# Performance work log

Measured on AMD Instinct MI355X. Metric: run time of the kernel, lower is better.

The kernel has to match this reference:

```python
import jax, jax.numpy as jnp
import numpy as np

B, C, H, W = 16, 64, 32, 32
E, HEADS, FF, L = 64, 4, 256, 3
NO_UNIT, INB = 6, 58
LN_EPS = 1e-5


def setup_inputs() -> dict:
    key = jax.random.key(0)
    ks = jax.random.split(key, 16)
    x = jax.random.normal(ks[0], (B, C, H, W), jnp.float32)
    # channel 58 = in-bounds everywhere; channel 6 = no-unit flag (Bernoulli 0.5)
    x = x.at[:, INB].set(1.0)
    x = x.at[:, NO_UNIT].set(jax.random.bernoulli(ks[1], 0.5, (B, H, W)).astype(jnp.float32))
    s = 0.05
    return {
        'x': x,
        'embed_w': jax.random.normal(ks[2], (C + 2, E), jnp.float32) * s,
        'embed_b': jnp.zeros((E,), jnp.float32),
        'ln1_w': jnp.ones((L, E), jnp.float32),
        'ln1_b': jnp.zeros((L, E), jnp.float32),
        'in_proj_w': jax.random.normal(ks[3], (L, 3 * E, E), jnp.float32) * s,
        'in_proj_b': jnp.zeros((L, 3 * E), jnp.float32),
        'out_w': jax.random.normal(ks[4], (L, E, E), jnp.float32) * s,
        'out_b': jnp.zeros((L, E), jnp.float32),
        'ln2_w': jnp.ones((L, E), jnp.float32),
        'ln2_b': jnp.zeros((L, E), jnp.float32),
        'ff1_w': jax.random.normal(ks[5], (L, E, FF), jnp.float32) * s,
        'ff1_b': jnp.zeros((L, FF), jnp.float32),
        'ff2_w': jax.random.normal(ks[6], (L, FF, E), jnp.float32) * s,
        'ff2_b': jnp.zeros((L, E), jnp.float32),
    }


def _layer_norm(x, w, b):
    mu = jnp.mean(x, axis=-1, keepdims=True)
    var = jnp.mean(jnp.square(x - mu), axis=-1, keepdims=True)
    return (x - mu) * jax.lax.rsqrt(var + LN_EPS) * w + b


def reference(x, embed_w, embed_b, ln1_w, ln1_b, in_proj_w, in_proj_b,
              out_w, out_b, ln2_w, ln2_b, ff1_w, ff1_b, ff2_w, ff2_b):
    Bn, Cn, Hn, Wn = x.shape
    S = Hn * Wn
    # position features (H == W here, matching torch tile/t() layout)
    ly = jnp.linspace(-1.0, 1.0, Hn)
    lx = jnp.linspace(-1.0, 1.0, Wn)
    pos = jnp.stack([jnp.tile(ly, (Wn, 1)), jnp.tile(lx, (Hn, 1)).T], axis=0)  # [2,H,W]
    xf = jnp.concatenate([x, jnp.broadcast_to(pos, (Bn, 2, Hn, Wn))], axis=1)
    xs = xf.reshape(Bn, Cn + 2, S).transpose(0, 2, 1)  # [B,S,C+2]

    # empty-space mask + vectorized squash (stable sort packs kept tokens first)
    empty = (xs[..., NO_UNIT] != 0) & (xs[..., INB] != 0)  # True = empty/masked
    keep = ~empty
    order = jnp.argsort(empty.astype(jnp.int32), axis=1, stable=True)  # [B,S]
    x_sq = jnp.take_along_axis(xs, order[:, :, None], axis=1)  # [B,S,C+2]
    n_keep = jnp.sum(keep, axis=1)
    pad = jnp.arange(S)[None, :] >= n_keep[:, None]  # True = padded key
    # (torch squashes to max(n_keep); padding to S is mathematically identical
    #  since padded rows are masked as keys and discarded on unsquash)
    bias = jnp.where(pad, -1e30, 0.0)[:, None, None, :]  # [B,1,1,S]

    h = x_sq @ embed_w + embed_b  # [B,S,E]
    dh = E // HEADS
    scale = 1.0 / float(np.sqrt(dh))
    for l in range(L):
        # identity_map_reordering: pre-norm attention
        a_in = _layer_norm(h, ln1_w[l], ln1_b[l])
        qkv = a_in @ in_proj_w[l].T + in_proj_b[l]
        q, k, v = jnp.split(qkv, 3, axis=-1)
        q = q.reshape(Bn, S, HEADS, dh)
        k = k.reshape(Bn, S, HEADS, dh)
        v = v.reshape(Bn, S, HEADS, dh)
        scores = jnp.einsum('bqhd,bkhd->bhqk', q, k) * scale + bias
        attn = jax.nn.softmax(scores, axis=-1)
        o = jnp.einsum('bhqk,bkhd->bqhd', attn, v).reshape(Bn, S, E)
        h = h + (o @ out_w[l].T + out_b[l])
        # pre-norm feed-forward (exact GELU, as nn.GELU default)
        f_in = _layer_norm(h, ln2_w[l], ln2_b[l])
        ff = jax.nn.gelu(f_in @ ff1_w[l] + ff1_b[l], approximate=False) @ ff2_w[l] + ff2_b[l]
        h = h + ff

    # unsquash: inverse permutation, zero at empty positions
    inv = jnp.argsort(order, axis=1)
    out = jnp.take_along_axis(h, inv[:, :, None], axis=1) * keep[:, :, None].astype(h.dtype)
    return out.transpose(0, 2, 1).reshape(Bn, E, Hn, Wn)
```

## Files before the change

kernel.cpp:

```cpp
#include <hip/hip_runtime.h>


#define BB 16
#define SS 1024
#define NT (BB*SS)

typedef short bf8 __attribute__((ext_vector_type(8)));
typedef float f4 __attribute__((ext_vector_type(4)));
typedef unsigned short u16;
typedef unsigned short us4 __attribute__((ext_vector_type(4)));

#define MFMA(a,b,c) __builtin_amdgcn_mfma_f32_16x16x32_bf16(a,b,c,0,0,0)

__device__ __forceinline__ float b2f(u16 u){
  union { unsigned int i; float f; } v; v.i = ((unsigned int)u) << 16; return v.f;
}
__device__ __forceinline__ u16 f2b(float f){
  union { float f; unsigned int i; } v; v.f = f;
  unsigned int x = v.i;
  return (u16)((x + 0x7FFFu + ((x >> 16) & 1u)) >> 16);
}
__device__ __forceinline__ int probe_f32(const void* ln1w){
  return ((const u16*)ln1w)[0] == 0;
}
__device__ __forceinline__ float ldf(const void* p, int i, int isf32){
  return isf32 ? ((const float*)p)[i] : b2f(((const u16*)p)[i]);
}
__device__ __forceinline__ bf8 ldbf8(const void* p, int idx, int isf32){
  if (!isf32) return *(const bf8*)((const u16*)p + idx);
  const float* s = (const float*)p + idx;
  bf8 r;
  #pragma unroll
  for (int j = 0; j < 8; j++) r[j] = (short)f2b(s[j]);
  return r;
}
__device__ __forceinline__ float gelu(float x){
  float y = 1.5957691216f * x * (1.f + 0.044715f * x * x);
  float e = __expf(y);
  return x - x * __builtin_amdgcn_rcpf(e + 1.f);
}

#define O_L1W  64
#define O_L1B  256
#define O_IPW  448
#define O_IPB  37312
#define O_OW   37888
#define O_OWB  50176
#define O_L2W  50368
#define O_L2B  50560
#define O_F1B  50752
#define O_F2B  51520

__device__ __forceinline__ void cv(u16* dst, const void* src, int n, int isf32,
                                   int tid, int nth){
  if (isf32){
    const float* s = (const float*)src;
    for (int i = tid; i < n; i += nth) dst[i] = f2b(s[i]);
  } else {
    const u16* s = (const u16*)src;
    for (int i = tid; i < n; i += nth) dst[i] = s[i];
  }
}

__device__ __forceinline__ void qkv_core(bf8 a0, bf8 a1, bf8 b0, bf8 b1,
    int j, float bj, int lane, int bb4, int sw,
    u16* __restrict__ qb, u16* __restrict__ kb, u16* __restrict__ vt)
{
  int quad = lane >> 4;
  f4 acc = {0.f,0.f,0.f,0.f};
  acc = MFMA(a0, b0, acc);
  acc = MFMA(a1, b1, acc);
  if (j < 128){
    u16* dst = (j < 64) ? qb : kb;
    int jj = j & 63; int hd = jj >> 4, d = jj & 15;
    int base = (bb4 + hd)*1024 + sw + quad*4;
    #pragma unroll
    for (int r = 0; r < 4; r++) dst[((base + r) << 4) + d] = f2b(acc[r] + bj);
  } else {
    int jj = j - 128; int hd = jj >> 4, d = jj & 15;
    us4 pk;
    #pragma unroll
    for (int r = 0; r < 4; r++) pk[r] = f2b(acc[r] + bj);
    *(us4*)(vt + ((bb4 + hd)*16 + d)*1024 + sw + quad*4) = pk;
  }
}

__device__ __forceinline__ void ln_to_lds(const f4* hf, int lane,
    const u16* __restrict__ w, const u16* __restrict__ bs, u16* als)
{
  int col = lane & 15, quad = lane >> 4;
  float sm[4], sq[4];
  #pragma unroll
  for (int r = 0; r < 4; r++){
    float a = 0.f, q2 = 0.f;
    #pragma unroll
    for (int f = 0; f < 4; f++){ float v = hf[f][r]; a += v; q2 += v*v; }
    sm[r] = a; sq[r] = q2;
  }
  #pragma unroll
  for (int off = 1; off < 16; off <<= 1){
    #pragma unroll
    for (int r = 0; r < 4; r++){
      sm[r] += __shfl_xor(sm[r], off, 64);
      sq[r] += __shfl_xor(sq[r], off, 64);
    }
  }
  #pragma unroll
  for (int r = 0; r < 4; r++){
    float m = sm[r] * 0.015625f;
    float rstd = rsqrtf(fmaxf(sq[r]*0.015625f - m*m, 0.f) + 1e-5f);
    sm[r] = m; sq[r] = rstd;
  }
  #pragma unroll
  for (int f = 0; f < 4; f++){
    int n = f*16 + col;
    float ww = b2f(w[n]), bb = b2f(bs[n]);
    #pragma unroll
    for (int r = 0; r < 4; r++)
      als[(quad*4 + r)*72 + n] = f2b((hf[f][r] - sm[r])*sq[r]*ww + bb);
  }
}

__device__ __forceinline__ void ln4(f4 val, int wave, int col, int quad,
    const u16* __restrict__ w, const u16* __restrict__ bs,
    u16* als, float (*lnred)[16][2])
{
  float sm[4], sq[4];
  #pragma unroll
  for (int r = 0; r < 4; r++){ sm[r] = val[r]; sq[r] = val[r]*val[r]; }
  #pragma unroll
  for (int off = 1; off < 16; off <<= 1){
    #pragma unroll
    for (int r = 0; r < 4; r++){
      sm[r] += __shfl_xor(sm[r], off, 64);
      sq[r] += __shfl_xor(sq[r], off, 64);
    }
  }
  if (col == 0){
    #pragma unroll
    for (int r = 0; r < 4; r++){
      lnred[wave][quad*4 + r][0] = sm[r];
      lnred[wave][quad*4 + r][1] = sq[r];
    }
  }
  __syncthreads();
  int n = wave*16 + col;
  float ww = b2f(w[n]), bb = b2f(bs[n]);
  #pragma unroll
  for (int r = 0; r < 4; r++){
    int row = quad*4 + r;
    float s0 = lnred[0][row][0] + lnred[1][row][0] + lnred[2][row][0] + lnred[3][row][0];
    float q0 = lnred[0][row][1] + lnred[1][row][1] + lnred[2][row][1] + lnred[3][row][1];
    float m = s0 * 0.015625f;
    float rs = rsqrtf(fmaxf(q0*0.015625f - m*m, 0.f) + 1e-5f);
    als[row*72 + n] = f2b((val[r] - m)*rs*ww + bb);
  }
}

__global__ __launch_bounds__(256) void k0(
    const void* __restrict__ x,    const void* __restrict__ ewS,
    const void* __restrict__ ebS,  const void* __restrict__ l1wS,
    const void* __restrict__ l1bS, const void* __restrict__ ipwS,
    const void* __restrict__ ipbS, const void* __restrict__ owS,
    const void* __restrict__ owbS, const void* __restrict__ l2wS,
    const void* __restrict__ l2bS, const void* __restrict__ f1wS,
    const void* __restrict__ f1bS, const void* __restrict__ f2wS,
    const void* __restrict__ f2bS,
    u16* __restrict__ cb, u16* __restrict__ f1t, u16* __restrict__ f2t,
    float* __restrict__ h, float* __restrict__ keepf,
    u16* __restrict__ qb, u16* __restrict__ kb, u16* __restrict__ vt)
{
  __shared__ __align__(16) u16 xs[4][16*104];
  __shared__ __align__(16) u16 als[4][16*72];
  __shared__ __align__(16) u16 ews[64*96];
  __shared__ __align__(16) u16 wsm[384];
  int tid = threadIdx.x;
  int lane = tid & 63, wave = tid >> 6;
  int col = lane & 15, quad = lane >> 4;
  int isf32 = probe_f32(l1wS);

  {
    int gtid = blockIdx.x*256 + tid;
    int nth  = gridDim.x*256;
    for (int i = gtid; i < 3*256*64; i += nth){
      int l = i / (256*64); int r = i % (256*64); int n = r / 64, k = r % 64;
      f1t[i] = f2b(ldf(f1wS, (l*64 + k)*256 + n, isf32));
    }
    for (int i = gtid; i < 3*64*256; i += nth){
      int l = i / (64*256); int r = i % (64*256); int n = r / 256, k = r % 256;
      f2t[i] = f2b(ldf(f2wS, (l*256 + k)*64 + n, isf32));
    }
    cv(cb + O_L1W, l1wS, 192,   isf32, gtid, nth);
    cv(cb + O_L1B, l1bS, 192,   isf32, gtid, nth);
    cv(cb + O_IPW, ipwS, 36864, isf32, gtid, nth);
    cv(cb + O_IPB, ipbS, 576,   isf32, gtid, nth);
    cv(cb + O_OW,  owS,  12288, isf32, gtid, nth);
    cv(cb + O_OWB, owbS, 192,   isf32, gtid, nth);
    cv(cb + O_L2W, l2wS, 192,   isf32, gtid, nth);
    cv(cb + O_L2B, l2bS, 192,   isf32, gtid, nth);
    cv(cb + O_F1B, f1bS, 768,   isf32, gtid, nth);
    cv(cb + O_F2B, f2bS, 192,   isf32, gtid, nth);
  }
  for (int i = tid; i < 64*96; i += 256){
    int n = i / 96, c = i - n*96;
    ews[i] = (c < 66) ? f2b(ldf(ewS, c*64 + n, isf32)) : (u16)0;
  }
  for (int i = tid; i < 384; i += 256){
    float v;
    if (i < 64)       v = ldf(ebS,  i,       isf32);
    else if (i < 128) v = ldf(l1wS, i - 64,  isf32);
    else if (i < 192) v = ldf(l1bS, i - 128, isf32);
    else              v = ldf(ipbS, i - 192, isf32);
    wsm[i] = f2b(v);
  }
  int t0 = blockIdx.x*64;
  int b = t0 >> 10;
  int tw = t0 + wave*16;
  int sw = (t0 & 1023) + wave*16;
  u16* axs = xs[wave];
  int s = sw + col;
  #pragma unroll
  for (int i = 0; i < 16; i++){
    int c = quad*16 + i;
    axs[col*104 + c] = f2b(ldf(x, ((b << 6) + c)*1024 + s, isf32));
  }
  #pragma unroll
  for (int i = 0; i < 8; i++){
    int c = 64 + quad*8 + i;
    float v = 0.f;
    if (c == 64)      v = -1.f + (2.f/31.f)*(float)(s & 31);
    else if (c == 65) v = -1.f + (2.f/31.f)*(float)((s >> 5) & 31);
    axs[col*104 + c] = f2b(v);
  }
  if (quad == 0){
    float x6  = ldf(x, ((b << 6) + 6)*1024 + s, isf32);
    float x58 = ldf(x, ((b << 6) + 58)*1024 + s, isf32);
    keepf[(b << 10) + s] = (x6 != 0.f && x58 != 0.f) ? 0.f : 1.f;
  }
  __syncthreads();
  bf8 af[3];
  #pragma unroll
  for (int kc = 0; kc < 3; kc++) af[kc] = *(const bf8*)(axs + col*104 + kc*32 + quad*8);
  f4 hf[4];
  #pragma unroll
  for (int f = 0; f < 4; f++){
    f4 acc = {0.f,0.f,0.f,0.f};
    #pragma unroll
    for (int kc = 0; kc < 3; kc++){
      bf8 bfr = *(const bf8*)(ews + (f*16+col)*96 + kc*32 + quad*8);
      acc = MFMA(af[kc], bfr, acc);
    }
    float bias = b2f(wsm[f*16 + col]);
    #pragma unroll
    for (int r = 0; r < 4; r++){
      acc[r] += bias;
      h[(tw + quad*4 + r)*64 + f*16 + col] = acc[r];
    }
    hf[f] = acc;
  }
  ln_to_lds(hf, lane, wsm + 64, wsm + 128, als[wave]);
  bf8 a0 = *(const bf8*)(als[wave] + col*72 + quad*8);
  bf8 a1 = *(const bf8*)(als[wave] + col*72 + 32 + quad*8);
  #pragma unroll
  for (int jt = 0; jt < 12; jt++){
    int j = jt*16 + col;
    bf8 b0 = ldbf8(ipwS, (jt*16+col)*64 + quad*8, isf32);
    bf8 b1 = ldbf8(ipwS, (jt*16+col)*64 + 32 + quad*8, isf32);
    qkv_core(a0, a1, b0, b1, j, b2f(wsm[192 + j]), lane, b << 2, sw, qb, kb, vt);
  }
}

__global__ __launch_bounds__(256) void k_layer(
    float* __restrict__ h, const u16* __restrict__ cb, int l, int nl,
    const u16* __restrict__ f1l, const u16* __restrict__ f2l,
    const u16* __restrict__ qbR, const u16* __restrict__ kbR,
    const u16* __restrict__ vtR,
    u16* __restrict__ qbW, u16* __restrict__ kbW, u16* __restrict__ vtW,
    const float* __restrict__ keepf, void* __restrict__ outp,
    const void* __restrict__ dtype_probe, int last)
{
  __shared__ __align__(16) u16 smem[6528];
  __shared__ float lnred[4][16][2];
  u16* plds = smem;
  u16* gls  = smem;
  u16* ols  = smem + 4224;
  u16* als  = smem + 5376;

  int tid = threadIdx.x;
  int lane = tid & 63, wave = tid >> 6;
  int col = lane & 15, quad = lane >> 4;
  int tile = blockIdx.x;
  int b = tile >> 6;
  int sw = (tile & 63) * 16;
  int tw = (b << 10) + sw;

  {
    int bh = (b << 2) + wave;
    const u16* qbase = qbR + (bh << 14);
    const u16* kbase = kbR + (bh << 14);
    const u16* vbase = vtR + (bh << 14);
    const float* kp = keepf + (b << 10);
    bf8 qf = {0,0,0,0,0,0,0,0};
    if (quad < 2) qf = *(const bf8*)(qbase + ((sw + col) << 4) + quad*8);
    f4 oacc = {0.f,0.f,0.f,0.f};
    float l4v[4] = {0.f,0.f,0.f,0.f};
    u16* pw = plds + wave*640;
    for (int kc = 0; kc < 1024; kc += 32){
      #pragma unroll
      for (int t = 0; t < 2; t++){
        bf8 kf = {0,0,0,0,0,0,0,0};
        int key = kc + t*16 + col;
        if (quad < 2) kf = *(const bf8*)(kbase + (key << 4) + quad*8);
        f4 sc = {0.f,0.f,0.f,0.f};
        sc = MFMA(qf, kf, sc);
        float kpv = kp[key];
        #pragma unroll
        for (int r = 0; r < 4; r++){
          float p = kpv * __expf(fminf(sc[r] * 0.25f, 60.f));
          l4v[r] += p;
          pw[(quad*4 + r)*40 + t*16 + col] = f2b(p);
        }
      }
      bf8 pf = *(const bf8*)(pw + col*40 + quad*8);
      bf8 vf = *(const bf8*)(vbase + col*1024 + kc + quad*8);
      oacc = MFMA(pf, vf, oacc);
    }
    #pragma unroll
    for (int off = 1; off < 16; off <<= 1)
      #pragma unroll
      for (int r = 0; r < 4; r++) l4v[r] += __shfl_xor(l4v[r], off, 64);
    #pragma unroll
    for (int r = 0; r < 4; r++){
      float rd = __builtin_amdgcn_rcpf(fmaxf(l4v[r], 1e-30f));
      ols[(quad*4 + r)*72 + wave*16 + col] = f2b(oacc[r] * rd);
    }
  }
  __syncthreads();

  {
    const u16* ow     = cb + O_OW  + l*4096;
    const u16* obias  = cb + O_OWB + l*64;
    const u16* f1b    = cb + O_F1B + l*256;
    const u16* f2bias = cb + O_F2B + l*64;
    int f = wave;
    bf8 af0 = *(const bf8*)(ols + col*72 + quad*8);
    bf8 af1 = *(const bf8*)(ols + col*72 + 32 + quad*8);
    f4 acc = {0.f,0.f,0.f,0.f};
    acc = MFMA(af0, *(const bf8*)(ow + (f*16+col)*64 + quad*8), acc);
    acc = MFMA(af1, *(const bf8*)(ow + (f*16+col)*64 + 32 + quad*8), acc);
    float bo = b2f(obias[f*16 + col]);
    f4 hfA;
    #pragma unroll
    for (int r = 0; r < 4; r++)
      hfA[r] = h[(tw + quad*4 + r)*64 + f*16 + col] + acc[r] + bo;
    ln4(hfA, wave, col, quad, cb + O_L2W + l*64, cb + O_L2B + l*64, als, lnred);
    __syncthreads();
    bf8 a0 = *(const bf8*)(als + col*72 + quad*8);
    bf8 a1 = *(const bf8*)(als + col*72 + 32 + quad*8);
    #pragma unroll
    for (int j = 0; j < 4; j++){
      int ft = wave*4 + j;
      f4 fa = {0.f,0.f,0.f,0.f};
      fa = MFMA(a0, *(const bf8*)(f1l + (ft*16+col)*64 + quad*8), fa);
      fa = MFMA(a1, *(const bf8*)(f1l + (ft*16+col)*64 + 32 + quad*8), fa);
      int n = ft*16 + col;
      float bb = b2f(f1b[n]);
      #pragma unroll
      for (int r = 0; r < 4; r++)
        gls[(quad*4 + r)*264 + n] = f2b(gelu(fa[r] + bb));
    }
    __syncthreads();
    bf8 gfr[8];
    #pragma unroll
    for (int kc = 0; kc < 8; kc++)
      gfr[kc] = *(const bf8*)(gls + col*264 + kc*32 + quad*8);
    f4 acc2 = {0.f,0.f,0.f,0.f};
    #pragma unroll
    for (int kc = 0; kc < 8; kc++)
      acc2 = MFMA(gfr[kc], *(const bf8*)(f2l + (f*16+col)*256 + kc*32 + quad*8), acc2);
    float b2v = b2f(f2bias[f*16 + col]);
    f4 hv;
    #pragma unroll
    for (int r = 0; r < 4; r++){
      float v = hfA[r] + acc2[r] + b2v;
      hv[r] = v;
      h[(tw + quad*4 + r)*64 + f*16 + col] = v;
    }
    if (last){
      int isf32 = probe_f32(dtype_probe);
      int bbq = tw >> 10, sbase = (tw & 1023) + quad*4;
      float kpr[4];
      #pragma unroll
      for (int r = 0; r < 4; r++) kpr[r] = keepf[tw + quad*4 + r];
      #pragma unroll
      for (int r = 0; r < 4; r++){
        float v = hv[r] * kpr[r];
        long idx = (long)((bbq << 6) + f*16 + col)*1024 + sbase + r;
        if (isf32) ((float*)outp)[idx] = v;
        else       ((u16*)outp)[idx]   = f2b(v);
      }
    } else {
      ln4(hv, wave, col, quad, cb + O_L1W + nl*64, cb + O_L1B + nl*64, als, lnred);
      __syncthreads();
      const u16* ipw = cb + O_IPW + nl*12288;
      const u16* ipb = cb + O_IPB + nl*192;
      bf8 qa0 = *(const bf8*)(als + col*72 + quad*8);
      bf8 qa1 = *(const bf8*)(als + col*72 + 32 + quad*8);
      #pragma unroll
      for (int j = 0; j < 3; j++){
        int jt = wave*3 + j;
        int jj = jt*16 + col;
        bf8 b0 = *(const bf8*)(ipw + (jt*16+col)*64 + quad*8);
        bf8 b1 = *(const bf8*)(ipw + (jt*16+col)*64 + 32 + quad*8);
        qkv_core(qa0, qa1, b0, b1, jj, b2f(ipb[jj]), lane, b << 2, sw,
                 qbW, kbW, vtW);
      }
    }
  }
}

extern "C" void kernel_launch(void* const* d_in, const int* in_sizes, int n_in,
                              void* d_out, int out_size, void* d_ws, size_t ws_size,
                              hipStream_t stream)
{
  (void)in_sizes; (void)n_in; (void)out_size; (void)ws_size;
  char* ws = (char*)d_ws;
  float* h     = (float*)(ws + 0);
  float* keepf = (float*)(ws + 4194304);
  u16*   qA    = (u16*)(ws + 4259840);
  u16*   kA    = (u16*)(ws + 6356992);
  u16*   vA    = (u16*)(ws + 8454144);
  u16*   qB    = (u16*)(ws + 10551296);
  u16*   kB    = (u16*)(ws + 12648448);
  u16*   vB    = (u16*)(ws + 14745600);
  u16*   f1t   = (u16*)(ws + 16842752);
  u16*   f2t   = (u16*)(ws + 16941056);
  u16*   cb    = (u16*)(ws + 17039360);

  k0<<<NT/64, 256, 0, stream>>>(d_in[0], d_in[1], d_in[2], d_in[3], d_in[4],
                                d_in[5], d_in[6], d_in[7], d_in[8], d_in[9],
                                d_in[10], d_in[11], d_in[12], d_in[13], d_in[14],
                                cb, f1t, f2t, h, keepf, qA, kA, vA);
  for (int l = 0; l < 3; l++){
    int nl = (l < 2) ? (l + 1) : 0;
    u16 *qR, *kR, *vR, *qW, *kW, *vW;
    if ((l & 1) == 0){ qR = qA; kR = kA; vR = vA; qW = qB; kW = kB; vW = vB; }
    else             { qR = qB; kR = kB; vR = vB; qW = qA; kW = kA; vW = vA; }
    k_layer<<<NT/16, 256, 0, stream>>>(h, cb, l, nl,
                                       f1t + l*16384, f2t + l*16384,
                                       qR, kR, vR, qW, kW, vW,
                                       keepf, d_out, d_in[3],
                                       (l == 2) ? 1 : 0);
  }
}
```

Before: 242.7 us.

## Compact kept tokens per batch and skip masked tokens in all layers

Each k0 block runs a prefix scan over the keep mask of its batch and builds a compacted index list of kept tokens plus a key-padding vector. Embedding, QKV and the per-layer blocks now run only on tiles that hold kept tokens, and the attention key loop stops at the kept count rounded up to 32. The final layer scatters results back to their original positions, and k0 zero-fills the output beforehand. This removes roughly half of the token and key work when about half the positions are empty, at the cost of a redundant scan in every block and an output memset.

After: 204.6 us. 1.19x faster.

```diff
diff --git a/kernel.cpp b/kernel.cpp
--- a/kernel.cpp
+++ b/kernel.cpp
@@ -167,17 +167,61 @@
     const void* __restrict__ f1bS, const void* __restrict__ f2wS,
     const void* __restrict__ f2bS,
     u16* __restrict__ cb, u16* __restrict__ f1t, u16* __restrict__ f2t,
-    float* __restrict__ h, float* __restrict__ keepf,
-    u16* __restrict__ qb, u16* __restrict__ kb, u16* __restrict__ vt)
+    float* __restrict__ h, int* __restrict__ nk, u16* __restrict__ cidx,
+    float* __restrict__ kpc,
+    u16* __restrict__ qb, u16* __restrict__ kb, u16* __restrict__ vt,
+    void* __restrict__ outp, int out_elems)
 {
   __shared__ __align__(16) u16 xs[4][16*104];
   __shared__ __align__(16) u16 als[4][16*72];
   __shared__ __align__(16) u16 ews[64*96];
   __shared__ __align__(16) u16 wsm[384];
+  __shared__ int scan[256];
+  __shared__ u16 lcidx[1024];
   int tid = threadIdx.x;
   int lane = tid & 63, wave = tid >> 6;
   int col = lane & 15, quad = lane >> 4;
   int isf32 = probe_f32(l1wS);
+  int b = blockIdx.x >> 4;
+  int seg = blockIdx.x & 15;
+
+  int kpl[4]; int c = 0;
+  #pragma unroll
+  for (int j = 0; j < 4; j++){
+    int s4 = tid*4 + j;
+    float x6  = ldf(x, ((b << 6) + 6)*1024 + s4, isf32);
+    float x58 = ldf(x, ((b << 6) + 58)*1024 + s4, isf32);
+    int k = (x6 != 0.f && x58 != 0.f) ? 0 : 1;
+    kpl[j] = k; c += k;
+  }
+  scan[tid] = c;
+  __syncthreads();
+  for (int off = 1; off < 256; off <<= 1){
+    int v = 0;
+    if (tid >= off) v = scan[tid - off];
+    __syncthreads();
+    scan[tid] += v;
+    __syncthreads();
+  }
+  int excl = scan[tid] - c;
+  int total = scan[255];
+  #pragma unroll
+  for (int j = 0; j < 4; j++) lcidx[tid*4 + j] = 0;
+  __syncthreads();
+  {
+    int p = excl;
+    #pragma unroll
+    for (int j = 0; j < 4; j++)
+      if (kpl[j]){ lcidx[p] = (u16)(tid*4 + j); p++; }
+  }
+  __syncthreads();
+  #pragma unroll
+  for (int j = 0; j < 4; j++){
+    int idx = tid*4 + j;
+    cidx[(b << 10) + idx] = lcidx[idx];
+    kpc[(b << 10) + idx]  = (idx < total) ? 1.f : 0.f;
+  }
+  if (tid == 0) nk[b] = total;
 
   {
     int gtid = blockIdx.x*256 + tid;
@@ -200,10 +244,13 @@
     cv(cb + O_L2B, l2bS, 192,   isf32, gtid, nth);
     cv(cb + O_F1B, f1bS, 768,   isf32, gtid, nth);
     cv(cb + O_F2B, f2bS, 192,   isf32, gtid, nth);
+    int words = isf32 ? out_elems : (out_elems >> 1);
+    unsigned int* op = (unsigned int*)outp;
+    for (int i = gtid; i < words; i += nth) op[i] = 0u;
   }
   for (int i = tid; i < 64*96; i += 256){
-    int n = i / 96, c = i - n*96;
-    ews[i] = (c < 66) ? f2b(ldf(ewS, c*64 + n, isf32)) : (u16)0;
+    int n = i / 96, cc = i - n*96;
+    ews[i] = (cc < 66) ? f2b(ldf(ewS, cc*64 + n, isf32)) : (u16)0;
   }
   for (int i = tid; i < 384; i += 256){
     float v;
@@ -213,31 +260,27 @@
     else              v = ldf(ipbS, i - 192, isf32);
     wsm[i] = f2b(v);
   }
-  int t0 = blockIdx.x*64;
-  int b = t0 >> 10;
-  int tw = t0 + wave*16;
-  int sw = (t0 & 1023) + wave*16;
+  __syncthreads();
+
+  int base = seg * 64;
+  if (base >= total) return;
+  int slot0 = base + wave*16;
+  int slotc = slot0 + col;
+  int s = lcidx[slotc];
   u16* axs = xs[wave];
-  int s = sw + col;
   #pragma unroll
   for (int i = 0; i < 16; i++){
-    int c = quad*16 + i;
-    axs[col*104 + c] = f2b(ldf(x, ((b << 6) + c)*1024 + s, isf32));
+    int cch = quad*16 + i;
+    axs[col*104 + cch] = f2b(ldf(x, ((b << 6) + cch)*1024 + s, isf32));
   }
   #pragma unroll
   for (int i = 0; i < 8; i++){
-    int c = 64 + quad*8 + i;
+    int cch = 64 + quad*8 + i;
     float v = 0.f;
-    if (c == 64)      v = -1.f + (2.f/31.f)*(float)(s & 31);
-    else if (c == 65) v = -1.f + (2.f/31.f)*(float)((s >> 5) & 31);
-    axs[col*104 + c] = f2b(v);
-  }
-  if (quad == 0){
-    float x6  = ldf(x, ((b << 6) + 6)*1024 + s, isf32);
-    float x58 = ldf(x, ((b << 6) + 58)*1024 + s, isf32);
-    keepf[(b << 10) + s] = (x6 != 0.f && x58 != 0.f) ? 0.f : 1.f;
-  }
-  __syncthreads();
+    if (cch == 64)      v = -1.f + (2.f/31.f)*(float)(s & 31);
+    else if (cch == 65) v = -1.f + (2.f/31.f)*(float)((s >> 5) & 31);
+    axs[col*104 + cch] = f2b(v);
+  }
   bf8 af[3];
   #pragma unroll
   for (int kc = 0; kc < 3; kc++) af[kc] = *(const bf8*)(axs + col*104 + kc*32 + quad*8);
@@ -254,7 +297,7 @@
     #pragma unroll
     for (int r = 0; r < 4; r++){
       acc[r] += bias;
-      h[(tw + quad*4 + r)*64 + f*16 + col] = acc[r];
+      h[((b << 10) + slot0 + quad*4 + r)*64 + f*16 + col] = acc[r];
     }
     hf[f] = acc;
   }
@@ -266,7 +309,7 @@
     int j = jt*16 + col;
     bf8 b0 = ldbf8(ipwS, (jt*16+col)*64 + quad*8, isf32);
     bf8 b1 = ldbf8(ipwS, (jt*16+col)*64 + 32 + quad*8, isf32);
-    qkv_core(a0, a1, b0, b1, j, b2f(wsm[192 + j]), lane, b << 2, sw, qb, kb, vt);
+    qkv_core(a0, a1, b0, b1, j, b2f(wsm[192 + j]), lane, b << 2, slot0, qb, kb, vt);
   }
 }
 
@@ -276,7 +319,8 @@
     const u16* __restrict__ qbR, const u16* __restrict__ kbR,
     const u16* __restrict__ vtR,
     u16* __restrict__ qbW, u16* __restrict__ kbW, u16* __restrict__ vtW,
-    const float* __restrict__ keepf, void* __restrict__ outp,
+    const int* __restrict__ nk, const u16* __restrict__ cidx,
+    const float* __restrict__ kpc, void* __restrict__ outp,
     const void* __restrict__ dtype_probe, int last)
 {
   __shared__ __align__(16) u16 smem[6528];
@@ -289,23 +333,25 @@
   int tid = threadIdx.x;
   int lane = tid & 63, wave = tid >> 6;
   int col = lane & 15, quad = lane >> 4;
-  int tile = blockIdx.x;
-  int b = tile >> 6;
-  int sw = (tile & 63) * 16;
-  int tw = (b << 10) + sw;
+  int b = blockIdx.x >> 6;
+  int tb = (blockIdx.x & 63) * 16;
+  int total = nk[b];
+  if (tb >= total) return;
+  int nk32 = (total + 31) & ~31;
+  int tw = (b << 10) + tb;
 
   {
     int bh = (b << 2) + wave;
     const u16* qbase = qbR + (bh << 14);
     const u16* kbase = kbR + (bh << 14);
     const u16* vbase = vtR + (bh << 14);
-    const float* kp = keepf + (b << 10);
+    const float* kp = kpc + (b << 10);
     bf8 qf = {0,0,0,0,0,0,0,0};
-    if (quad < 2) qf = *(const bf8*)(qbase + ((sw + col) << 4) + quad*8);
+    if (quad < 2) qf = *(const bf8*)(qbase + ((tb + col) << 4) + quad*8);
     f4 oacc = {0.f,0.f,0.f,0.f};
     float l4v[4] = {0.f,0.f,0.f,0.f};
     u16* pw = plds + wave*640;
-    for (int kc = 0; kc < 1024; kc += 32){
+    for (int kc = 0; kc < nk32; kc += 32){
       #pragma unroll
       for (int t = 0; t < 2; t++){
         bf8 kf = {0,0,0,0,0,0,0,0};
@@ -388,16 +434,15 @@
     }
     if (last){
       int isf32 = probe_f32(dtype_probe);
-      int bbq = tw >> 10, sbase = (tw & 1023) + quad*4;
-      float kpr[4];
-      #pragma unroll
-      for (int r = 0; r < 4; r++) kpr[r] = keepf[tw + quad*4 + r];
       #pragma unroll
       for (int r = 0; r < 4; r++){
-        float v = hv[r] * kpr[r];
-        long idx = (long)((bbq << 6) + f*16 + col)*1024 + sbase + r;
-        if (isf32) ((float*)outp)[idx] = v;
-        else       ((u16*)outp)[idx]   = f2b(v);
+        int slot = tb + quad*4 + r;
+        if (slot < total){
+          int s = cidx[(b << 10) + slot];
+          long idx = (long)((b << 6) + f*16 + col)*1024 + s;
+          if (isf32) ((float*)outp)[idx] = hv[r];
+          else       ((u16*)outp)[idx]   = f2b(hv[r]);
+        }
       }
     } else {
       ln4(hv, wave, col, quad, cb + O_L1W + nl*64, cb + O_L1B + nl*64, als, lnred);
@@ -412,7 +457,7 @@
         int jj = jt*16 + col;
         bf8 b0 = *(const bf8*)(ipw + (jt*16+col)*64 + quad*8);
         bf8 b1 = *(const bf8*)(ipw + (jt*16+col)*64 + 32 + quad*8);
-        qkv_core(qa0, qa1, b0, b1, jj, b2f(ipb[jj]), lane, b << 2, sw,
+        qkv_core(qa0, qa1, b0, b1, jj, b2f(ipb[jj]), lane, b << 2, tb,
                  qbW, kbW, vtW);
       }
     }
@@ -423,24 +468,27 @@
                               void* d_out, int out_size, void* d_ws, size_t ws_size,
                               hipStream_t stream)
 {
-  (void)in_sizes; (void)n_in; (void)out_size; (void)ws_size;
+  (void)in_sizes; (void)n_in; (void)ws_size;
   char* ws = (char*)d_ws;
   float* h     = (float*)(ws + 0);
-  float* keepf = (float*)(ws + 4194304);
-  u16*   qA    = (u16*)(ws + 4259840);
-  u16*   kA    = (u16*)(ws + 6356992);
-  u16*   vA    = (u16*)(ws + 8454144);
-  u16*   qB    = (u16*)(ws + 10551296);
-  u16*   kB    = (u16*)(ws + 12648448);
-  u16*   vB    = (u16*)(ws + 14745600);
-  u16*   f1t   = (u16*)(ws + 16842752);
-  u16*   f2t   = (u16*)(ws + 16941056);
-  u16*   cb    = (u16*)(ws + 17039360);
+  int*   nk    = (int*)(ws + 4194304);
+  u16*   cidx  = (u16*)(ws + 4194368);
+  float* kpc   = (float*)(ws + 4227136);
+  u16*   qA    = (u16*)(ws + 4292672);
+  u16*   kA    = (u16*)(ws + 6389824);
+  u16*   vA    = (u16*)(ws + 8486976);
+  u16*   qB    = (u16*)(ws + 10584128);
+  u16*   kB    = (u16*)(ws + 12681280);
+  u16*   vB    = (u16*)(ws + 14778432);
+  u16*   f1t   = (u16*)(ws + 16875584);
+  u16*   f2t   = (u16*)(ws + 16973888);
+  u16*   cb    = (u16*)(ws + 17072192);
 
   k0<<<NT/64, 256, 0, stream>>>(d_in[0], d_in[1], d_in[2], d_in[3], d_in[4],
                                 d_in[5], d_in[6], d_in[7], d_in[8], d_in[9],
                                 d_in[10], d_in[11], d_in[12], d_in[13], d_in[14],
-                                cb, f1t, f2t, h, keepf, qA, kA, vA);
+                                cb, f1t, f2t, h, nk, cidx, kpc,
+                                qA, kA, vA, d_out, out_size);
   for (int l = 0; l < 3; l++){
     int nl = (l < 2) ? (l + 1) : 0;
     u16 *qR, *kR, *vR, *qW, *kW, *vW;
@@ -449,7 +497,7 @@
     k_layer<<<NT/16, 256, 0, stream>>>(h, cb, l, nl,
                                        f1t + l*16384, f2t + l*16384,
                                        qR, kR, vR, qW, kW, vW,
-                                       keepf, d_out, d_in[3],
+                                       nk, cidx, kpc, d_out, d_in[3],
                                        (l == 2) ? 1 : 0);
   }
 }
```
